# Kernel tuning notes

Hardware: AMD Instinct MI355X
Metric: run time of the kernel (lower is better)

## Reference

```python
import jax, jax.numpy as jnp
import numpy as np


def _average(x, w, W):
    """layers.Average forward: weighted mean over batch of Linear(x) (bias=False).
    x: [N, d_in], w: [N, 1], W: [d_out, d_in] -> [1, d_out]"""
    h = x @ W.T                                    # [N, d_out]
    return jnp.sum(h * w, axis=0, keepdims=True) / jnp.sum(w)


def setup_inputs() -> dict:
    key = jax.random.key(0)
    k1, k2, k3, k4 = jax.random.split(key, 4)
    N, n_in, n_middle = 1_000_000, 32, 128
    x = jax.random.normal(k1, (N, n_in), dtype=jnp.float32)
    w = jax.random.uniform(k2, (N, 1), dtype=jnp.float32)
    # Linear weights (Kaiming-ish scale), bias=False per __init__ default
    W_in = jax.random.normal(k3, (n_middle, n_in), dtype=jnp.float32) / np.float32(np.sqrt(n_in))
    W_out = jax.random.normal(k4, (n_in, n_middle), dtype=jnp.float32) / np.float32(np.sqrt(n_middle))
    return {"x": x, "w": w, "W_in": W_in, "W_out": W_out}


def reference(x, w, W_in, W_out):
    # x_ = activation(avg_in(x, w))
    h = jax.nn.relu(_average(x, w, W_in))          # [1, n_middle]
    # x_ = avg_out(x_, w); residual add (broadcast over batch)
    x_ = _average(h, w, W_out)                     # [1, n_in]
    return x + x_                                  # [N, n_in]
```

## Files before the change

kernel.cpp:

```cpp
#include <hip/hip_runtime.h>

#define BS 256
#define NB1 1024
#define NB3 2048

__global__ void __launch_bounds__(BS) reduce_kernel(
    const float* __restrict__ x, const float* __restrict__ w,
    float* __restrict__ colpart, float* __restrict__ wpart, long long total4) {
  const int tid = threadIdx.x;
  const long long stride = (long long)gridDim.x * BS;
  const float4* x4 = (const float4*)x;
  float4 acc = make_float4(0.f, 0.f, 0.f, 0.f);
  float wacc = 0.f;
  const bool is_w = ((tid & 7) == 0);
  for (long long c = (long long)blockIdx.x * BS + tid; c < total4; c += stride) {
    const int row = (int)(c >> 3);
    const float wi = w[row];
    const float4 v = x4[c];
    acc.x = fmaf(wi, v.x, acc.x);
    acc.y = fmaf(wi, v.y, acc.y);
    acc.z = fmaf(wi, v.z, acc.z);
    acc.w = fmaf(wi, v.w, acc.w);
    if (is_w) wacc += wi;
  }
  __shared__ float4 sacc[BS];
  __shared__ float  sw[BS];
  sacc[tid] = acc;
  sw[tid] = wacc;
  __syncthreads();
  for (int s = BS / 2; s >= 8; s >>= 1) {
    if (tid < s) {
      float4 o = sacc[tid + s];
      sacc[tid].x += o.x; sacc[tid].y += o.y;
      sacc[tid].z += o.z; sacc[tid].w += o.w;
      sw[tid] += sw[tid + s];
    }
    __syncthreads();
  }
  if (tid < 8) {
    ((float4*)(colpart + (long long)blockIdx.x * 32))[tid] = sacc[tid];
  }
  if (tid == 0) {
    float wsum = sw[0] + sw[1] + sw[2] + sw[3] + sw[4] + sw[5] + sw[6] + sw[7];
    wpart[blockIdx.x] = wsum;
  }
}

__global__ void __launch_bounds__(BS) middle_kernel(
    const float* __restrict__ colpart, const float* __restrict__ wpart,
    const float* __restrict__ W_in, const float* __restrict__ W_out,
    float* __restrict__ r_out, int nb) {
  __shared__ float red[BS];
  __shared__ float wred[BS];
  __shared__ float avg[32];
  __shared__ float h[128];
  const int tid = threadIdx.x;
  {
    const int col = tid & 31, grp = tid >> 5;
    float s = 0.f;
    for (int b = grp; b < nb; b += 8) s += colpart[b * 32 + col];
    red[tid] = s;
  }
  {
    float s = 0.f;
    for (int b = tid; b < nb; b += BS) s += wpart[b];
    wred[tid] = s;
  }
  __syncthreads();
  for (int s = BS / 2; s >= 1; s >>= 1) {
    if (tid < s) wred[tid] += wred[tid + s];
    __syncthreads();
  }
  if (tid < 32) {
    float s = 0.f;
    for (int g = 0; g < 8; ++g) s += red[tid + 32 * g];
    avg[tid] = s / wred[0];
  }
  __syncthreads();
  if (tid < 128) {
    float a = 0.f;
    for (int k = 0; k < 32; ++k) a = fmaf(W_in[tid * 32 + k], avg[k], a);
    h[tid] = fmaxf(a, 0.f);
  }
  __syncthreads();
  if (tid < 32) {
    float r = 0.f;
    for (int k = 0; k < 128; ++k) r = fmaf(W_out[tid * 128 + k], h[k], r);
    r_out[tid] = r;
  }
}

__global__ void __launch_bounds__(BS) add_kernel(
    const float* __restrict__ x, const float* __restrict__ r,
    float* __restrict__ out, long long total4) {
  const int tid = threadIdx.x;
  __shared__ float4 rs[8];
  if (tid < 8) rs[tid] = ((const float4*)r)[tid];
  __syncthreads();
  const float4 rr = rs[tid & 7];
  const long long stride = (long long)gridDim.x * BS;
  const float4* x4 = (const float4*)x;
  float4* o4 = (float4*)out;
  for (long long c = (long long)blockIdx.x * BS + tid; c < total4; c += stride) {
    float4 v = x4[c];
    v.x += rr.x; v.y += rr.y; v.z += rr.z; v.w += rr.w;
    o4[c] = v;
  }
}

extern "C" void kernel_launch(void* const* d_in, const int* in_sizes, int n_in,
                              void* d_out, int out_size, void* d_ws, size_t ws_size,
                              hipStream_t stream) {
  const float* x     = (const float*)d_in[0];
  const float* w     = (const float*)d_in[1];
  const float* W_in  = (const float*)d_in[2];
  const float* W_out = (const float*)d_in[3];
  float* out = (float*)d_out;

  const long long N = (long long)in_sizes[0] / 32;
  const long long total4 = N * 8;

  int nb = NB1;
  while (nb > 64 && (size_t)(nb * 33 + 32) * 4 > ws_size) nb >>= 1;
  float* colpart = (float*)d_ws;
  float* wpart   = colpart + (size_t)nb * 32;
  float* r       = wpart + nb;

  reduce_kernel<<<nb, BS, 0, stream>>>(x, w, colpart, wpart, total4);
  middle_kernel<<<1, BS, 0, stream>>>(colpart, wpart, W_in, W_out, r, nb);
  add_kernel<<<NB3, BS, 0, stream>>>(x, r, out, total4);
}
```

Before: 280.9 us.

## Unroll reduce/add loops 2x, use nontemporal stores, vectorize middle reduction

Both streaming kernels now process two float4 chunks per iteration with independent accumulators, which raises memory-level parallelism. The reduce grid doubles to 2048 blocks. The add kernel writes its output with nontemporal stores so the 128MB write bypasses the cache, and it reads r directly without a shared-memory sync. The middle kernel now reduces the partials with float4 loads, and the weight sum is now accumulated by every lane and then scaled by 1/8 to correct for the duplication.

```diff
diff --git a/kernel.cpp b/kernel.cpp
--- a/kernel.cpp
+++ b/kernel.cpp
@@ -1,48 +1,55 @@
 #include <hip/hip_runtime.h>
 
 #define BS 256
-#define NB1 1024
+#define NB1 2048
 #define NB3 2048
+
+typedef float vfloat4 __attribute__((ext_vector_type(4)));
 
 __global__ void __launch_bounds__(BS) reduce_kernel(
     const float* __restrict__ x, const float* __restrict__ w,
     float* __restrict__ colpart, float* __restrict__ wpart, long long total4) {
   const int tid = threadIdx.x;
-  const long long stride = (long long)gridDim.x * BS;
-  const float4* x4 = (const float4*)x;
-  float4 acc = make_float4(0.f, 0.f, 0.f, 0.f);
-  float wacc = 0.f;
-  const bool is_w = ((tid & 7) == 0);
-  for (long long c = (long long)blockIdx.x * BS + tid; c < total4; c += stride) {
-    const int row = (int)(c >> 3);
-    const float wi = w[row];
-    const float4 v = x4[c];
-    acc.x = fmaf(wi, v.x, acc.x);
-    acc.y = fmaf(wi, v.y, acc.y);
-    acc.z = fmaf(wi, v.z, acc.z);
-    acc.w = fmaf(wi, v.w, acc.w);
-    if (is_w) wacc += wi;
+  const long long stride2 = (long long)gridDim.x * (2 * BS);
+  const vfloat4* x4 = (const vfloat4*)x;
+  vfloat4 a0 = (vfloat4)(0.f);
+  vfloat4 a1 = (vfloat4)(0.f);
+  float w0 = 0.f, w1 = 0.f;
+  long long c = (long long)blockIdx.x * (2 * BS) + tid;
+  for (; c + BS < total4; c += stride2) {
+    const float wi0 = w[(int)(c >> 3)];
+    const float wi1 = w[(int)((c + BS) >> 3)];
+    const vfloat4 v0 = x4[c];
+    const vfloat4 v1 = x4[c + BS];
+    a0 += wi0 * v0;
+    a1 += wi1 * v1;
+    w0 += wi0; w1 += wi1;
   }
-  __shared__ float4 sacc[BS];
-  __shared__ float  sw[BS];
-  sacc[tid] = acc;
-  sw[tid] = wacc;
+  if (c < total4) {
+    const float wi = w[(int)(c >> 3)];
+    a0 += wi * x4[c];
+    w0 += wi;
+  }
+  a0 += a1;
+  w0 += w1;
+  __shared__ vfloat4 sacc[BS];
+  __shared__ float   sw[BS];
+  sacc[tid] = a0;
+  sw[tid] = w0;
   __syncthreads();
   for (int s = BS / 2; s >= 8; s >>= 1) {
     if (tid < s) {
-      float4 o = sacc[tid + s];
-      sacc[tid].x += o.x; sacc[tid].y += o.y;
-      sacc[tid].z += o.z; sacc[tid].w += o.w;
+      sacc[tid] += sacc[tid + s];
       sw[tid] += sw[tid + s];
     }
     __syncthreads();
   }
   if (tid < 8) {
-    ((float4*)(colpart + (long long)blockIdx.x * 32))[tid] = sacc[tid];
+    ((vfloat4*)(colpart + (long long)blockIdx.x * 32))[tid] = sacc[tid];
   }
   if (tid == 0) {
-    float wsum = sw[0] + sw[1] + sw[2] + sw[3] + sw[4] + sw[5] + sw[6] + sw[7];
-    wpart[blockIdx.x] = wsum;
+    wpart[blockIdx.x] = sw[0] + sw[1] + sw[2] + sw[3] +
+                        sw[4] + sw[5] + sw[6] + sw[7];
   }
 }
 
@@ -50,31 +57,45 @@
     const float* __restrict__ colpart, const float* __restrict__ wpart,
     const float* __restrict__ W_in, const float* __restrict__ W_out,
     float* __restrict__ r_out, int nb) {
-  __shared__ float red[BS];
-  __shared__ float wred[BS];
-  __shared__ float avg[32];
-  __shared__ float h[128];
   const int tid = threadIdx.x;
+  __shared__ vfloat4 sacc[BS];
+  __shared__ float   swr[BS];
+  __shared__ float   avg[32];
+  __shared__ float   h[128];
   {
-    const int col = tid & 31, grp = tid >> 5;
-    float s = 0.f;
-    for (int b = grp; b < nb; b += 8) s += colpart[b * 32 + col];
-    red[tid] = s;
+    const vfloat4* cp4 = (const vfloat4*)colpart;
+    const int nchunk = nb * 8;
+    vfloat4 acc = (vfloat4)(0.f);
+    for (int cb = tid; cb < nchunk; cb += BS) acc += cp4[cb];
+    sacc[tid] = acc;
   }
   {
+    const vfloat4* wp4 = (const vfloat4*)wpart;
+    const int nchunk = nb / 4;
     float s = 0.f;
-    for (int b = tid; b < nb; b += BS) s += wpart[b];
-    wred[tid] = s;
+    for (int cb = tid; cb < nchunk; cb += BS) {
+      vfloat4 v = wp4[cb];
+      s += v.x + v.y + v.z + v.w;
+    }
+    swr[tid] = s;
   }
   __syncthreads();
-  for (int s = BS / 2; s >= 1; s >>= 1) {
-    if (tid < s) wred[tid] += wred[tid + s];
+  for (int s = BS / 2; s >= 8; s >>= 1) {
+    if (tid < s) {
+      sacc[tid] += sacc[tid + s];
+      swr[tid] += swr[tid + s];
+    }
     __syncthreads();
   }
+  if (tid == 0) {
+    float wsum = (swr[0] + swr[1] + swr[2] + swr[3] +
+                  swr[4] + swr[5] + swr[6] + swr[7]) * 0.125f;
+    swr[0] = wsum;
+  }
+  __syncthreads();
   if (tid < 32) {
-    float s = 0.f;
-    for (int g = 0; g < 8; ++g) s += red[tid + 32 * g];
-    avg[tid] = s / wred[0];
+    const float* sflat = (const float*)sacc;
+    avg[tid] = sflat[tid] / swr[0];
   }
   __syncthreads();
   if (tid < 128) {
@@ -94,17 +115,20 @@
     const float* __restrict__ x, const float* __restrict__ r,
     float* __restrict__ out, long long total4) {
   const int tid = threadIdx.x;
-  __shared__ float4 rs[8];
-  if (tid < 8) rs[tid] = ((const float4*)r)[tid];
-  __syncthreads();
-  const float4 rr = rs[tid & 7];
-  const long long stride = (long long)gridDim.x * BS;
-  const float4* x4 = (const float4*)x;
-  float4* o4 = (float4*)out;
-  for (long long c = (long long)blockIdx.x * BS + tid; c < total4; c += stride) {
-    float4 v = x4[c];
-    v.x += rr.x; v.y += rr.y; v.z += rr.z; v.w += rr.w;
-    o4[c] = v;
+  const vfloat4 rr = ((const vfloat4*)r)[tid & 7];
+  const long long stride2 = (long long)gridDim.x * (2 * BS);
+  const vfloat4* x4 = (const vfloat4*)x;
+  vfloat4* o4 = (vfloat4*)out;
+  long long c = (long long)blockIdx.x * (2 * BS) + tid;
+  for (; c + BS < total4; c += stride2) {
+    vfloat4 v0 = x4[c] + rr;
+    vfloat4 v1 = x4[c + BS] + rr;
+    __builtin_nontemporal_store(v0, &o4[c]);
+    __builtin_nontemporal_store(v1, &o4[c + BS]);
+  }
+  if (c < total4) {
+    vfloat4 v = x4[c] + rr;
+    __builtin_nontemporal_store(v, &o4[c]);
   }
 }
 
```

New measurement: 265.5 us. -5.5%, faster.
